# Performance work log

Hardware: AMD Instinct MI355X
Metric: run time of the kernel (lower is better)

## Reference

```python
import jax, jax.numpy as jnp
import numpy as np

N_NODES = 50000
N_EDGES = 800000
IN_DIM, HID_DIM, OUT_DIM = 128, 128, 64


def setup_inputs() -> dict:
    key = jax.random.key(0)
    ks = jax.random.split(key, 8)
    x = jax.random.normal(ks[0], (N_NODES, IN_DIM), dtype=jnp.float32)
    edge_index = jax.random.randint(ks[1], (2, N_EDGES), 0, N_NODES, dtype=jnp.int64)
    # GCNConv uses Glorot weights + zero bias; any random init is fine for a reference
    W1 = jax.random.normal(ks[2], (IN_DIM, HID_DIM), dtype=jnp.float32) / np.sqrt(IN_DIM)
    b1 = jnp.zeros((HID_DIM,), dtype=jnp.float32)
    W2 = jax.random.normal(ks[3], (HID_DIM, OUT_DIM), dtype=jnp.float32) / np.sqrt(HID_DIM)
    b2 = jnp.zeros((OUT_DIM,), dtype=jnp.float32)
    Wfc = jax.random.normal(ks[4], (OUT_DIM, 2), dtype=jnp.float32) / np.sqrt(OUT_DIM)
    bfc = jnp.zeros((2,), dtype=jnp.float32)
    return {"x": x, "edge_index": edge_index, "W1": W1, "b1": b1,
            "W2": W2, "b2": b2, "Wfc": Wfc, "bfc": bfc}


def _gcn_conv(x, src, dst, W, b, n_nodes):
    """PyG GCNConv: out = D^{-1/2} (A+I) D^{-1/2} (x W) + b."""
    xw = x @ W  # [N, F_out] transform before propagation
    ones = jnp.ones(src.shape[0], dtype=xw.dtype)
    deg = jax.ops.segment_sum(ones, dst, num_segments=n_nodes) + 1.0  # +1 for self-loop
    dinv = jax.lax.rsqrt(deg)
    norm = dinv[src] * dinv[dst]  # [E]
    msg = xw[src] * norm[:, None]  # gather + scale: [E, F_out]
    agg = jax.ops.segment_sum(msg, dst, num_segments=n_nodes)  # scatter-add
    agg = agg + xw * (dinv * dinv)[:, None]  # self-loop contribution (norm = 1/deg)
    return agg + b


def reference(x, edge_index, W1, b1, W2, b2, Wfc, bfc):
    n = x.shape[0]
    src, dst = edge_index[0], edge_index[1]
    h = jax.nn.relu(_gcn_conv(x, src, dst, W1, b1, n))
    # dropout is identity in eval mode
    h = _gcn_conv(h, src, dst, W2, b2, n)
    h = h @ Wfc + bfc
    return jax.nn.leaky_relu(h, negative_slope=0.01)
```

## Files before the change

kernel.cpp:

```cpp
#include <hip/hip_runtime.h>
#include <hip/hip_fp16.h>

#define IN_DIM 128
#define HID_DIM 128
#define OUT_DIM 64
#define BINW 128
#define BINSHIFT 7
#define MAXBIN 512
#define CAP 4096
#define CNTSTRIDE 16
#define SC_GRID 512
#define SBUF 2176

typedef _Float16 f16x8 __attribute__((ext_vector_type(8)));
typedef float f32x4 __attribute__((ext_vector_type(4)));

__global__ __launch_bounds__(256) void k_build_gemm(const float* __restrict__ x,
                                                    const float* __restrict__ W,
                                                    __half* __restrict__ xwh,
                                                    const int* __restrict__ src,
                                                    const int* __restrict__ dst,
                                                    int* __restrict__ bin_cnt,
                                                    int* __restrict__ ovf_cnt,
                                                    unsigned int* __restrict__ ovf,
                                                    unsigned int* __restrict__ ebin,
                                                    int N, int E, int nbin) {
    __shared__ union SMem {
        unsigned int wt_raw[8192];
        struct {
            int h[MAXBIN];
            int excl[MAXBIN];
            int base_s[MAXBIN];
            int ps[256];
            unsigned int sb1[SBUF];
            unsigned int sb2[SBUF];
        } sc;
    } smem;
    const int nGemm = (N + 127) >> 7;
    int tid = threadIdx.x;

    if ((int)blockIdx.x < nGemm) {
        char* wb = (char*)smem.wt_raw;
        {
            int kk0 = (tid & 15) * 2;
            int c8  = (tid >> 4) * 8;
#pragma unroll
            for (int i = 0; i < 4; ++i) {
                int kk = i * 32 + kk0;
                const float* w0 = W + (size_t)kk * HID_DIM + c8;
                const float* w1 = w0 + HID_DIM;
                float4 a0 = *(const float4*)w0;
                float4 a1 = *(const float4*)(w0 + 4);
                float4 b0 = *(const float4*)w1;
                float4 b1 = *(const float4*)(w1 + 4);
                float va[8] = {a0.x, a0.y, a0.z, a0.w, a1.x, a1.y, a1.z, a1.w};
                float vb[8] = {b0.x, b0.y, b0.z, b0.w, b1.x, b1.y, b1.z, b1.w};
#pragma unroll
                for (int j = 0; j < 8; ++j) {
                    int col = c8 + j;
                    int byte = (col << 8) + (kk << 1);
                    byte ^= ((col & 7) << 4);
                    *(__half2*)(wb + byte) = __floats2half2_rn(va[j], vb[j]);
                }
            }
        }
        int lane = tid & 63;
        int wv   = tid >> 6;
        int lcol = lane & 15;
        int lk   = (lane >> 4) << 3;
        int swz  = (lcol & 7) << 4;
        int rb   = blockIdx.x * 128 + wv * 32;
        int rows[2];
        const float* xp[2];
#pragma unroll
        for (int r = 0; r < 2; ++r) {
            int row = rb + 16 * r + lcol;
            rows[r] = row;
            if (row > N - 1) row = N - 1;
            xp[r] = x + (size_t)row * IN_DIM + lk;
        }
        f32x4 acc[2][8];
#pragma unroll
        for (int r = 0; r < 2; ++r)
#pragma unroll
            for (int c = 0; c < 8; ++c) acc[r][c] = (f32x4){0.f, 0.f, 0.f, 0.f};

        __syncthreads();

        auto mk = [](float4 f0, float4 f1, f16x8& hi, f16x8& lo) {
            float f[8] = {f0.x, f0.y, f0.z, f0.w, f1.x, f1.y, f1.z, f1.w};
#pragma unroll
            for (int e = 0; e < 8; ++e) {
                _Float16 h = (_Float16)f[e];
                hi[e] = h;
                lo[e] = (_Float16)(f[e] - (float)h);
            }
        };
#pragma unroll
        for (int kc = 0; kc < 4; ++kc) {
            f16x8 xhi[2], xlo[2];
#pragma unroll
            for (int r = 0; r < 2; ++r) {
                float4 f0 = *(const float4*)(xp[r] + kc * 32);
                float4 f1 = *(const float4*)(xp[r] + kc * 32 + 4);
                mk(f0, f1, xhi[r], xlo[r]);
            }
#pragma unroll
            for (int c = 0; c < 8; ++c) {
                int ad = ((c << 12) | (lcol << 8) | ((kc << 6) + (lk << 1))) ^ swz;
                f16x8 wfrag = *(const f16x8*)(wb + ad);
                acc[0][c] = __builtin_amdgcn_mfma_f32_16x16x32_f16(wfrag, xhi[0], acc[0][c], 0, 0, 0);
                acc[0][c] = __builtin_amdgcn_mfma_f32_16x16x32_f16(wfrag, xlo[0], acc[0][c], 0, 0, 0);
                acc[1][c] = __builtin_amdgcn_mfma_f32_16x16x32_f16(wfrag, xhi[1], acc[1][c], 0, 0, 0);
                acc[1][c] = __builtin_amdgcn_mfma_f32_16x16x32_f16(wfrag, xlo[1], acc[1][c], 0, 0, 0);
            }
        }
        int cq = lane >> 4;
#pragma unroll
        for (int r = 0; r < 2; ++r) {
            if (rows[r] < N) {
                uint2* p = (uint2*)(xwh + (size_t)rows[r] * HID_DIM);
#pragma unroll
                for (int c = 0; c < 8; ++c) {
                    union { __half2 h[2]; uint2 u; } pk;
                    pk.h[0] = __floats2half2_rn(acc[r][c].x, acc[r][c].y);
                    pk.h[1] = __floats2half2_rn(acc[r][c].z, acc[r][c].w);
                    p[4 * c + cq] = pk.u;
                }
            }
        }
    } else {
        int sb = blockIdx.x - nGemm;
        int* h = smem.sc.h;
        int* excl = smem.sc.excl;
        int* base_s = smem.sc.base_s;
        int* ps = smem.sc.ps;
        unsigned int* sb1 = smem.sc.sb1;
        unsigned int* sb2 = smem.sc.sb2;
        for (int k = tid; k < MAXBIN; k += 256) h[k] = 0;
        __syncthreads();
        int per = E / SC_GRID;
        int ebeg = sb * per;
        int eend = (sb + 1 == SC_GRID) ? E : ebeg + per;
        for (int i = ebeg + tid; i < eend; i += 256) {
            unsigned int s = (unsigned int)src[i];
            unsigned int d = (unsigned int)dst[i];
            sb1[i - ebeg] = s | (d << 16);
            atomicAdd(&h[d >> BINSHIFT], 1);
        }
        __syncthreads();
        int b0 = 2 * tid, b1 = 2 * tid + 1;
        int c0 = h[b0], c1 = h[b1];
        ps[tid] = c0 + c1;
        __syncthreads();
        for (int off = 1; off < 256; off <<= 1) {
            int v = (tid >= off) ? ps[tid - off] : 0;
            __syncthreads();
            ps[tid] += v;
            __syncthreads();
        }
        int Pprev = (tid > 0) ? ps[tid - 1] : 0;
        excl[b0] = Pprev;
        excl[b1] = Pprev + c0;
        __syncthreads();
        for (int k = tid; k < nbin; k += 256) {
            int c = h[k];
            base_s[k] = (c > 0) ? atomicAdd(&bin_cnt[k * CNTSTRIDE], c) : 0;
            h[k] = 0;
        }
        __syncthreads();
        int tot = eend - ebeg;
        for (int i = tid; i < tot; i += 256) {
            unsigned int p = sb1[i];
            int b = (int)(p >> (16 + BINSHIFT));
            int r = atomicAdd(&h[b], 1);
            sb2[excl[b] + r] = p;
        }
        __syncthreads();
        for (int i = tid; i < tot; i += 256) {
            unsigned int p = sb2[i];
            int b = (int)(p >> (16 + BINSHIFT));
            int g = base_s[b] + (i - excl[b]);
            if (g < CAP) ebin[(size_t)b * CAP + g] = p;
            else ovf[atomicAdd(ovf_cnt, 1)] = p;
        }
    }
}

__global__ __launch_bounds__(256) void k_fill(const unsigned int* __restrict__ ebin,
                                              const int* __restrict__ bin_cnt,
                                              const int* __restrict__ ovf_cnt,
                                              const unsigned int* __restrict__ ovf,
                                              int* __restrict__ row_ptr,
                                              unsigned short* __restrict__ degu,
                                              unsigned short* __restrict__ csr_src,
                                              float* __restrict__ dinv,
                                              const float* __restrict__ W2,
                                              const float* __restrict__ Wfc,
                                              const float* __restrict__ b2,
                                              const float* __restrict__ bfc,
                                              float* __restrict__ Wc,
                                              float* __restrict__ bc,
                                              int N, int nbin) {
    __shared__ int cnt[BINW];
    __shared__ int excl[BINW];
    __shared__ int start[BINW];
    __shared__ unsigned int segl[CAP];
    int k = blockIdx.x;
    int node0 = k * BINW;
    int nn = min(BINW, N - node0);
    int t = threadIdx.x;
    if (t < BINW) cnt[t] = 0;
    int cnt_k = min(bin_cnt[k * CNTSTRIDE], CAP);
    const unsigned int* seg = ebin + (size_t)k * CAP;
    for (int i = t; i < cnt_k; i += 256) segl[i] = seg[i];
    __syncthreads();
    for (int i = t; i < cnt_k; i += 256)
        atomicAdd(&cnt[(segl[i] >> 16) & (BINW - 1)], 1);
    int novf = *ovf_cnt;
    for (int i = t; i < novf; i += 256) {
        unsigned int e = ovf[i];
        if ((int)(e >> (16 + BINSHIFT)) == k)
            atomicAdd(&cnt[(e >> 16) & (BINW - 1)], 1);
    }
    __syncthreads();
    if (t < BINW) excl[t] = (t < nn) ? cnt[t] : 0;
    __syncthreads();
    for (int off = 1; off < BINW; off <<= 1) {
        int u = 0;
        if (t < BINW && t >= off) u = excl[t - off];
        __syncthreads();
        if (t < BINW) excl[t] += u;
        __syncthreads();
    }
    if (t < nn) {
        int deg = cnt[t];
        int e0 = k * CAP + excl[t] - deg;
        start[t] = e0;
        row_ptr[node0 + t] = e0;
        degu[node0 + t] = (unsigned short)deg;
        dinv[node0 + t] = rsqrtf((float)deg + 1.0f);
        cnt[t] = 0;
    }
    __syncthreads();
    for (int i = t; i < cnt_k; i += 256) {
        unsigned int e = segl[i];
        int dl = (e >> 16) & (BINW - 1);
        int slot = start[dl] + atomicAdd(&cnt[dl], 1);
        csr_src[slot] = (unsigned short)(e & 0xffffu);
    }
    for (int i = t; i < novf; i += 256) {
        unsigned int e = ovf[i];
        if ((int)(e >> (16 + BINSHIFT)) == k) {
            int dl = (e >> 16) & (BINW - 1);
            int slot = start[dl] + atomicAdd(&cnt[dl], 1);
            csr_src[slot] = (unsigned short)(e & 0xffffu);
        }
    }
    if (k == 0) {
        int kk = t >> 1, j = t & 1;
        float acc = 0.f;
#pragma unroll 8
        for (int m = 0; m < OUT_DIM; ++m) acc += W2[kk * OUT_DIM + m] * Wfc[m * 2 + j];
        Wc[kk * 2 + j] = acc;
        if (kk == 0) {
            float b = 0.f;
#pragma unroll 8
            for (int m = 0; m < OUT_DIM; ++m) b += b2[m] * Wfc[m * 2 + j];
            bc[j] = b + bfc[j];
        }
    }
}

__global__ __launch_bounds__(256) void k_agg1z(const int* __restrict__ row_ptr,
                                               const unsigned short* __restrict__ degu,
                                               const unsigned short* __restrict__ csr_src,
                                               const float* __restrict__ dinv,
                                               const __half* __restrict__ xwh,
                                               const float* __restrict__ b1,
                                               const float* __restrict__ Wc,
                                               float* __restrict__ z, int N) {
    constexpr int F = HID_DIM;
    constexpr int L = F / 8;
    constexpr int EPW = 64 / L;
    __shared__ float Wcs[HID_DIM * 2];
    int tid = threadIdx.x;
    if (tid < 64) ((float4*)Wcs)[tid] = ((const float4*)Wc)[tid];
    __syncthreads();
    int node = (blockIdx.x * 256 + tid) >> 6;
    if (node >= N) return;
    int lane = tid & 63;
    int sub = lane / L;
    int c   = lane % L;
    int beg = row_ptr[node];
    int end = beg + degu[node];
    float dd = dinv[node];
    uint4 us = *(const uint4*)(xwh + (size_t)node * F + c * 8);
    float4 b1a = *(const float4*)(b1 + c * 8);
    float4 b1b = *(const float4*)(b1 + c * 8 + 4);
    float a0 = 0.f, a1 = 0.f, a2 = 0.f, a3 = 0.f;
    float a4 = 0.f, a5 = 0.f, a6 = 0.f, a7 = 0.f;
    auto acc = [&](uint4 u, float w) {
        float2 v0 = __half22float2(*(__half2*)&u.x);
        float2 v1 = __half22float2(*(__half2*)&u.y);
        float2 v2 = __half22float2(*(__half2*)&u.z);
        float2 v3 = __half22float2(*(__half2*)&u.w);
        a0 = fmaf(v0.x, w, a0); a1 = fmaf(v0.y, w, a1);
        a2 = fmaf(v1.x, w, a2); a3 = fmaf(v1.y, w, a3);
        a4 = fmaf(v2.x, w, a4); a5 = fmaf(v2.y, w, a5);
        a6 = fmaf(v3.x, w, a6); a7 = fmaf(v3.y, w, a7);
    };
    int j = beg + sub;
    for (; j + 3 * EPW < end; j += 4 * EPW) {
        int s0 = csr_src[j];
        int s1 = csr_src[j + EPW];
        int s2 = csr_src[j + 2 * EPW];
        int s3 = csr_src[j + 3 * EPW];
        uint4 u0 = *(const uint4*)(xwh + (size_t)s0 * F + c * 8);
        uint4 u1 = *(const uint4*)(xwh + (size_t)s1 * F + c * 8);
        uint4 u2 = *(const uint4*)(xwh + (size_t)s2 * F + c * 8);
        uint4 u3 = *(const uint4*)(xwh + (size_t)s3 * F + c * 8);
        float w0 = dinv[s0];
        float w1 = dinv[s1];
        float w2 = dinv[s2];
        float w3 = dinv[s3];
        acc(u0, w0); acc(u1, w1); acc(u2, w2); acc(u3, w3);
    }
    for (; j < end; j += EPW) {
        int s = csr_src[j];
        uint4 u = *(const uint4*)(xwh + (size_t)s * F + c * 8);
        acc(u, dinv[s]);
    }
#pragma unroll
    for (int off = L; off < 64; off <<= 1) {
        a0 += __shfl_xor(a0, off); a1 += __shfl_xor(a1, off);
        a2 += __shfl_xor(a2, off); a3 += __shfl_xor(a3, off);
        a4 += __shfl_xor(a4, off); a5 += __shfl_xor(a5, off);
        a6 += __shfl_xor(a6, off); a7 += __shfl_xor(a7, off);
    }
    float2 v0 = __half22float2(*(__half2*)&us.x);
    float2 v1 = __half22float2(*(__half2*)&us.y);
    float2 v2 = __half22float2(*(__half2*)&us.z);
    float2 v3 = __half22float2(*(__half2*)&us.w);
    float h[8];
    h[0] = fmaxf(fmaf(fmaf(v0.x, dd, a0), dd, b1a.x), 0.f);
    h[1] = fmaxf(fmaf(fmaf(v0.y, dd, a1), dd, b1a.y), 0.f);
    h[2] = fmaxf(fmaf(fmaf(v1.x, dd, a2), dd, b1a.z), 0.f);
    h[3] = fmaxf(fmaf(fmaf(v1.y, dd, a3), dd, b1a.w), 0.f);
    h[4] = fmaxf(fmaf(fmaf(v2.x, dd, a4), dd, b1b.x), 0.f);
    h[5] = fmaxf(fmaf(fmaf(v2.y, dd, a5), dd, b1b.y), 0.f);
    h[6] = fmaxf(fmaf(fmaf(v3.x, dd, a6), dd, b1b.z), 0.f);
    h[7] = fmaxf(fmaf(fmaf(v3.y, dd, a7), dd, b1b.w), 0.f);
    float o0 = 0.f, o1 = 0.f;
#pragma unroll
    for (int k = 0; k < 8; ++k) {
        o0 += h[k] * Wcs[(c * 8 + k) * 2 + 0];
        o1 += h[k] * Wcs[(c * 8 + k) * 2 + 1];
    }
#pragma unroll
    for (int off = 1; off < L; off <<= 1) {
        o0 += __shfl_xor(o0, off);
        o1 += __shfl_xor(o1, off);
    }
    if (lane == 0) {
        float2 r; r.x = o0 * dd; r.y = o1 * dd;
        *(float2*)(z + (size_t)node * 2) = r;
    }
}

__global__ __launch_bounds__(256) void k_agg2(const int* __restrict__ row_ptr,
                                              const unsigned short* __restrict__ degu,
                                              const unsigned short* __restrict__ csr_src,
                                              const float* __restrict__ dinv,
                                              const float* __restrict__ z,
                                              const float* __restrict__ bc,
                                              float* __restrict__ out, int N) {
    int tid = threadIdx.x;
    int gwave = (blockIdx.x * 256 + tid) >> 6;
    int lane = tid & 63;
    int grp = lane >> 3, li = lane & 7;
    int node = gwave * 8 + grp;
    if (node >= N) return;
    int beg = row_ptr[node];
    int end = beg + degu[node];
    float s0 = 0.f, s1 = 0.f;
    int j = beg + li;
    for (; j + 8 < end; j += 16) {
        int sa = csr_src[j];
        int sb = csr_src[j + 8];
        float2 za = *(const float2*)(z + (size_t)sa * 2);
        float2 zb = *(const float2*)(z + (size_t)sb * 2);
        s0 += za.x + zb.x; s1 += za.y + zb.y;
    }
    if (j < end) {
        int s = csr_src[j];
        float2 zv = *(const float2*)(z + (size_t)s * 2);
        s0 += zv.x; s1 += zv.y;
    }
#pragma unroll
    for (int off = 1; off < 8; off <<= 1) {
        s0 += __shfl_xor(s0, off);
        s1 += __shfl_xor(s1, off);
    }
    if (li == 0) {
        float2 zs = *(const float2*)(z + (size_t)node * 2);
        float dd = dinv[node];
        float o0 = (s0 + zs.x) * dd + bc[0];
        float o1 = (s1 + zs.y) * dd + bc[1];
        float2 r;
        r.x = o0 > 0.f ? o0 : 0.01f * o0;
        r.y = o1 > 0.f ? o1 : 0.01f * o1;
        *(float2*)(out + (size_t)node * 2) = r;
    }
}

extern "C" void kernel_launch(void* const* d_in, const int* in_sizes, int n_in,
                              void* d_out, int out_size, void* d_ws, size_t ws_size,
                              hipStream_t stream) {
    const float* x   = (const float*)d_in[0];
    const int*   ei  = (const int*)d_in[1];
    const float* W1  = (const float*)d_in[2];
    const float* b1  = (const float*)d_in[3];
    const float* W2  = (const float*)d_in[4];
    const float* b2  = (const float*)d_in[5];
    const float* Wfc = (const float*)d_in[6];
    const float* bfc = (const float*)d_in[7];

    const int N = in_sizes[0] / IN_DIM;
    const int E = in_sizes[1] / 2;
    const int* src = ei;
    const int* dst = ei + E;
    const int nbin = (N + BINW - 1) / BINW;

    char* base = (char*)d_ws;
    size_t off = 0;
    auto take = [&](size_t bytes) { size_t o = off; off = (off + bytes + 255) & ~(size_t)255; return (void*)(base + o); };
    int*    row_ptr  = (int*)take((size_t)N * 4);
    unsigned short* degu = (unsigned short*)take((size_t)N * 2);
    unsigned short* csr_src = (unsigned short*)take((size_t)nbin * CAP * 2);
    int*    bin_cnt  = (int*)take((size_t)(nbin * CNTSTRIDE + CNTSTRIDE) * 4);
    int*    ovf_cnt  = bin_cnt + nbin * CNTSTRIDE;
    unsigned int* ovf = (unsigned int*)take((size_t)E * 4);
    unsigned int* ebin = (unsigned int*)take((size_t)nbin * CAP * 4);
    float*  dinv     = (float*)take((size_t)N * 4);
    __half* xw1h     = (__half*)take((size_t)N * HID_DIM * 2);
    float*  zbuf     = (float*)take((size_t)N * 2 * 4);
    float*  Wc       = (float*)take((size_t)HID_DIM * 2 * 4);
    float*  bc       = (float*)take(2 * 4);

    hipMemsetAsync(bin_cnt, 0, (size_t)(nbin * CNTSTRIDE + CNTSTRIDE) * 4, stream);

    const int nGemm = (N + 127) / 128;
    k_build_gemm<<<nGemm + SC_GRID, 256, 0, stream>>>(x, W1, xw1h, src, dst, bin_cnt,
                                                      ovf_cnt, ovf, ebin, N, E, nbin);
    k_fill<<<nbin, 256, 0, stream>>>(ebin, bin_cnt, ovf_cnt, ovf, row_ptr, degu,
                                     csr_src, dinv, W2, Wfc, b2, bfc, Wc, bc, N, nbin);
    k_agg1z<<<(N + 3) / 4, 256, 0, stream>>>(row_ptr, degu, csr_src, dinv, xw1h, b1, Wc, zbuf, N);
    const int nAgg2 = ((N + 7) / 8 * 64 + 255) / 256;
    k_agg2<<<nAgg2, 256, 0, stream>>>(row_ptr, degu, csr_src, dinv, zbuf, bc, (float*)d_out, N);
}
```

Measured before the change: 159.1 us.

## Fuse CSR fill with layer-1 aggregation and compute degrees via global atomics

```diff
diff --git a/kernel.cpp b/kernel.cpp
--- a/kernel.cpp
+++ b/kernel.cpp
@@ -9,8 +9,8 @@
 #define MAXBIN 512
 #define CAP 4096
 #define CNTSTRIDE 16
-#define SC_GRID 512
-#define SBUF 2176
+#define SC_GRID 256
+#define SBUF 3456
 
 typedef _Float16 f16x8 __attribute__((ext_vector_type(8)));
 typedef float f32x4 __attribute__((ext_vector_type(4)));
@@ -24,6 +24,7 @@
                                                     int* __restrict__ ovf_cnt,
                                                     unsigned int* __restrict__ ovf,
                                                     unsigned int* __restrict__ ebin,
+                                                    int* __restrict__ deg,
                                                     int N, int E, int nbin) {
     __shared__ union SMem {
         unsigned int wt_raw[8192];
@@ -147,6 +148,7 @@
             unsigned int d = (unsigned int)dst[i];
             sb1[i - ebeg] = s | (d << 16);
             atomicAdd(&h[d >> BINSHIFT], 1);
+            atomicAdd(&deg[d], 1);
         }
         __syncthreads();
         int b0 = 2 * tid, b1 = 2 * tid + 1;
@@ -187,25 +189,30 @@
     }
 }
 
-__global__ __launch_bounds__(256) void k_fill(const unsigned int* __restrict__ ebin,
-                                              const int* __restrict__ bin_cnt,
-                                              const int* __restrict__ ovf_cnt,
-                                              const unsigned int* __restrict__ ovf,
-                                              int* __restrict__ row_ptr,
-                                              unsigned short* __restrict__ degu,
-                                              unsigned short* __restrict__ csr_src,
-                                              float* __restrict__ dinv,
-                                              const float* __restrict__ W2,
-                                              const float* __restrict__ Wfc,
-                                              const float* __restrict__ b2,
-                                              const float* __restrict__ bfc,
-                                              float* __restrict__ Wc,
-                                              float* __restrict__ bc,
-                                              int N, int nbin) {
+__global__ __launch_bounds__(256) void k_fillagg(const unsigned int* __restrict__ ebin,
+                                                 const int* __restrict__ bin_cnt,
+                                                 const int* __restrict__ ovf_cnt,
+                                                 const unsigned int* __restrict__ ovf,
+                                                 const int* __restrict__ deg,
+                                                 int* __restrict__ row_ptr,
+                                                 unsigned short* __restrict__ degu,
+                                                 unsigned short* __restrict__ csr_src,
+                                                 float* __restrict__ dinv,
+                                                 const __half* __restrict__ xwh,
+                                                 const float* __restrict__ b1,
+                                                 const float* __restrict__ W2,
+                                                 const float* __restrict__ Wfc,
+                                                 const float* __restrict__ b2,
+                                                 const float* __restrict__ bfc,
+                                                 float* __restrict__ bc,
+                                                 float* __restrict__ z,
+                                                 int N, int nbin) {
     __shared__ int cnt[BINW];
     __shared__ int excl[BINW];
-    __shared__ int start[BINW];
+    __shared__ int start_s[BINW];
     __shared__ unsigned int segl[CAP];
+    __shared__ unsigned short csrl[CAP];
+    __shared__ float Wcs[HID_DIM * 2];
     int k = blockIdx.x;
     int node0 = k * BINW;
     int nn = min(BINW, N - node0);
@@ -214,6 +221,19 @@
     int cnt_k = min(bin_cnt[k * CNTSTRIDE], CAP);
     const unsigned int* seg = ebin + (size_t)k * CAP;
     for (int i = t; i < cnt_k; i += 256) segl[i] = seg[i];
+    {
+        int kk = t >> 1, j = t & 1;
+        float acc = 0.f;
+#pragma unroll 8
+        for (int m = 0; m < OUT_DIM; ++m) acc += W2[kk * OUT_DIM + m] * Wfc[m * 2 + j];
+        Wcs[kk * 2 + j] = acc;
+        if (k == 0 && kk == 0) {
+            float b = 0.f;
+#pragma unroll 8
+            for (int m = 0; m < OUT_DIM; ++m) b += b2[m] * Wfc[m * 2 + j];
+            bc[j] = b + bfc[j];
+        }
+    }
     __syncthreads();
     for (int i = t; i < cnt_k; i += 256)
         atomicAdd(&cnt[(segl[i] >> 16) & (BINW - 1)], 1);
@@ -234,137 +254,117 @@
         __syncthreads();
     }
     if (t < nn) {
-        int deg = cnt[t];
-        int e0 = k * CAP + excl[t] - deg;
-        start[t] = e0;
-        row_ptr[node0 + t] = e0;
-        degu[node0 + t] = (unsigned short)deg;
-        dinv[node0 + t] = rsqrtf((float)deg + 1.0f);
+        int d = cnt[t];
+        int e0 = excl[t] - d;
+        start_s[t] = e0;
+        row_ptr[node0 + t] = k * CAP + e0;
+        degu[node0 + t] = (unsigned short)d;
+        dinv[node0 + t] = rsqrtf((float)d + 1.0f);
         cnt[t] = 0;
     }
     __syncthreads();
     for (int i = t; i < cnt_k; i += 256) {
         unsigned int e = segl[i];
         int dl = (e >> 16) & (BINW - 1);
-        int slot = start[dl] + atomicAdd(&cnt[dl], 1);
-        csr_src[slot] = (unsigned short)(e & 0xffffu);
+        int slot = start_s[dl] + atomicAdd(&cnt[dl], 1);
+        unsigned short sv = (unsigned short)(e & 0xffffu);
+        csrl[slot] = sv;
+        csr_src[(size_t)k * CAP + slot] = sv;
     }
     for (int i = t; i < novf; i += 256) {
         unsigned int e = ovf[i];
         if ((int)(e >> (16 + BINSHIFT)) == k) {
             int dl = (e >> 16) & (BINW - 1);
-            int slot = start[dl] + atomicAdd(&cnt[dl], 1);
-            csr_src[slot] = (unsigned short)(e & 0xffffu);
-        }
-    }
-    if (k == 0) {
-        int kk = t >> 1, j = t & 1;
-        float acc = 0.f;
-#pragma unroll 8
-        for (int m = 0; m < OUT_DIM; ++m) acc += W2[kk * OUT_DIM + m] * Wfc[m * 2 + j];
-        Wc[kk * 2 + j] = acc;
-        if (kk == 0) {
-            float b = 0.f;
-#pragma unroll 8
-            for (int m = 0; m < OUT_DIM; ++m) b += b2[m] * Wfc[m * 2 + j];
-            bc[j] = b + bfc[j];
-        }
-    }
-}
-
-__global__ __launch_bounds__(256) void k_agg1z(const int* __restrict__ row_ptr,
-                                               const unsigned short* __restrict__ degu,
-                                               const unsigned short* __restrict__ csr_src,
-                                               const float* __restrict__ dinv,
-                                               const __half* __restrict__ xwh,
-                                               const float* __restrict__ b1,
-                                               const float* __restrict__ Wc,
-                                               float* __restrict__ z, int N) {
-    constexpr int F = HID_DIM;
-    constexpr int L = F / 8;
-    constexpr int EPW = 64 / L;
-    __shared__ float Wcs[HID_DIM * 2];
-    int tid = threadIdx.x;
-    if (tid < 64) ((float4*)Wcs)[tid] = ((const float4*)Wc)[tid];
+            int slot = start_s[dl] + atomicAdd(&cnt[dl], 1);
+            unsigned short sv = (unsigned short)(e & 0xffffu);
+            csrl[slot] = sv;
+            csr_src[(size_t)k * CAP + slot] = sv;
+        }
+    }
     __syncthreads();
-    int node = (blockIdx.x * 256 + tid) >> 6;
-    if (node >= N) return;
-    int lane = tid & 63;
-    int sub = lane / L;
-    int c   = lane % L;
-    int beg = row_ptr[node];
-    int end = beg + degu[node];
-    float dd = dinv[node];
-    uint4 us = *(const uint4*)(xwh + (size_t)node * F + c * 8);
-    float4 b1a = *(const float4*)(b1 + c * 8);
-    float4 b1b = *(const float4*)(b1 + c * 8 + 4);
-    float a0 = 0.f, a1 = 0.f, a2 = 0.f, a3 = 0.f;
-    float a4 = 0.f, a5 = 0.f, a6 = 0.f, a7 = 0.f;
-    auto acc = [&](uint4 u, float w) {
-        float2 v0 = __half22float2(*(__half2*)&u.x);
-        float2 v1 = __half22float2(*(__half2*)&u.y);
-        float2 v2 = __half22float2(*(__half2*)&u.z);
-        float2 v3 = __half22float2(*(__half2*)&u.w);
-        a0 = fmaf(v0.x, w, a0); a1 = fmaf(v0.y, w, a1);
-        a2 = fmaf(v1.x, w, a2); a3 = fmaf(v1.y, w, a3);
-        a4 = fmaf(v2.x, w, a4); a5 = fmaf(v2.y, w, a5);
-        a6 = fmaf(v3.x, w, a6); a7 = fmaf(v3.y, w, a7);
-    };
-    int j = beg + sub;
-    for (; j + 3 * EPW < end; j += 4 * EPW) {
-        int s0 = csr_src[j];
-        int s1 = csr_src[j + EPW];
-        int s2 = csr_src[j + 2 * EPW];
-        int s3 = csr_src[j + 3 * EPW];
-        uint4 u0 = *(const uint4*)(xwh + (size_t)s0 * F + c * 8);
-        uint4 u1 = *(const uint4*)(xwh + (size_t)s1 * F + c * 8);
-        uint4 u2 = *(const uint4*)(xwh + (size_t)s2 * F + c * 8);
-        uint4 u3 = *(const uint4*)(xwh + (size_t)s3 * F + c * 8);
-        float w0 = dinv[s0];
-        float w1 = dinv[s1];
-        float w2 = dinv[s2];
-        float w3 = dinv[s3];
-        acc(u0, w0); acc(u1, w1); acc(u2, w2); acc(u3, w3);
-    }
-    for (; j < end; j += EPW) {
-        int s = csr_src[j];
-        uint4 u = *(const uint4*)(xwh + (size_t)s * F + c * 8);
-        acc(u, dinv[s]);
-    }
-#pragma unroll
-    for (int off = L; off < 64; off <<= 1) {
-        a0 += __shfl_xor(a0, off); a1 += __shfl_xor(a1, off);
-        a2 += __shfl_xor(a2, off); a3 += __shfl_xor(a3, off);
-        a4 += __shfl_xor(a4, off); a5 += __shfl_xor(a5, off);
-        a6 += __shfl_xor(a6, off); a7 += __shfl_xor(a7, off);
-    }
-    float2 v0 = __half22float2(*(__half2*)&us.x);
-    float2 v1 = __half22float2(*(__half2*)&us.y);
-    float2 v2 = __half22float2(*(__half2*)&us.z);
-    float2 v3 = __half22float2(*(__half2*)&us.w);
-    float h[8];
-    h[0] = fmaxf(fmaf(fmaf(v0.x, dd, a0), dd, b1a.x), 0.f);
-    h[1] = fmaxf(fmaf(fmaf(v0.y, dd, a1), dd, b1a.y), 0.f);
-    h[2] = fmaxf(fmaf(fmaf(v1.x, dd, a2), dd, b1a.z), 0.f);
-    h[3] = fmaxf(fmaf(fmaf(v1.y, dd, a3), dd, b1a.w), 0.f);
-    h[4] = fmaxf(fmaf(fmaf(v2.x, dd, a4), dd, b1b.x), 0.f);
-    h[5] = fmaxf(fmaf(fmaf(v2.y, dd, a5), dd, b1b.y), 0.f);
-    h[6] = fmaxf(fmaf(fmaf(v3.x, dd, a6), dd, b1b.z), 0.f);
-    h[7] = fmaxf(fmaf(fmaf(v3.y, dd, a7), dd, b1b.w), 0.f);
-    float o0 = 0.f, o1 = 0.f;
-#pragma unroll
-    for (int k = 0; k < 8; ++k) {
-        o0 += h[k] * Wcs[(c * 8 + k) * 2 + 0];
-        o1 += h[k] * Wcs[(c * 8 + k) * 2 + 1];
-    }
-#pragma unroll
-    for (int off = 1; off < L; off <<= 1) {
-        o0 += __shfl_xor(o0, off);
-        o1 += __shfl_xor(o1, off);
-    }
-    if (lane == 0) {
-        float2 r; r.x = o0 * dd; r.y = o1 * dd;
-        *(float2*)(z + (size_t)node * 2) = r;
+    int lane = t & 63;
+    int wv4 = t >> 6;
+    int sub = lane >> 4;
+    int c = lane & 15;
+    for (int p = 0; p < BINW / 4; ++p) {
+        int nl = p * 4 + wv4;
+        if (nl >= nn) continue;
+        int node = node0 + nl;
+        int beg = start_s[nl];
+        int dcnt = cnt[nl];
+        int end = beg + dcnt;
+        float dd = rsqrtf((float)dcnt + 1.0f);
+        uint4 us = *(const uint4*)(xwh + (size_t)node * HID_DIM + c * 8);
+        float4 b1a = *(const float4*)(b1 + c * 8);
+        float4 b1b = *(const float4*)(b1 + c * 8 + 4);
+        float a0 = 0.f, a1 = 0.f, a2 = 0.f, a3 = 0.f;
+        float a4 = 0.f, a5 = 0.f, a6 = 0.f, a7 = 0.f;
+        auto accf = [&](uint4 u, float w) {
+            float2 v0 = __half22float2(*(__half2*)&u.x);
+            float2 v1 = __half22float2(*(__half2*)&u.y);
+            float2 v2 = __half22float2(*(__half2*)&u.z);
+            float2 v3 = __half22float2(*(__half2*)&u.w);
+            a0 = fmaf(v0.x, w, a0); a1 = fmaf(v0.y, w, a1);
+            a2 = fmaf(v1.x, w, a2); a3 = fmaf(v1.y, w, a3);
+            a4 = fmaf(v2.x, w, a4); a5 = fmaf(v2.y, w, a5);
+            a6 = fmaf(v3.x, w, a6); a7 = fmaf(v3.y, w, a7);
+        };
+        int j = beg + sub;
+        for (; j + 12 < end; j += 16) {
+            int s0 = csrl[j];
+            int s1 = csrl[j + 4];
+            int s2 = csrl[j + 8];
+            int s3 = csrl[j + 12];
+            uint4 u0 = *(const uint4*)(xwh + (size_t)s0 * HID_DIM + c * 8);
+            uint4 u1 = *(const uint4*)(xwh + (size_t)s1 * HID_DIM + c * 8);
+            uint4 u2 = *(const uint4*)(xwh + (size_t)s2 * HID_DIM + c * 8);
+            uint4 u3 = *(const uint4*)(xwh + (size_t)s3 * HID_DIM + c * 8);
+            float w0 = rsqrtf((float)deg[s0] + 1.0f);
+            float w1 = rsqrtf((float)deg[s1] + 1.0f);
+            float w2 = rsqrtf((float)deg[s2] + 1.0f);
+            float w3 = rsqrtf((float)deg[s3] + 1.0f);
+            accf(u0, w0); accf(u1, w1); accf(u2, w2); accf(u3, w3);
+        }
+        for (; j < end; j += 4) {
+            int s = csrl[j];
+            uint4 u = *(const uint4*)(xwh + (size_t)s * HID_DIM + c * 8);
+            accf(u, rsqrtf((float)deg[s] + 1.0f));
+        }
+#pragma unroll
+        for (int off = 16; off < 64; off <<= 1) {
+            a0 += __shfl_xor(a0, off); a1 += __shfl_xor(a1, off);
+            a2 += __shfl_xor(a2, off); a3 += __shfl_xor(a3, off);
+            a4 += __shfl_xor(a4, off); a5 += __shfl_xor(a5, off);
+            a6 += __shfl_xor(a6, off); a7 += __shfl_xor(a7, off);
+        }
+        float2 v0 = __half22float2(*(__half2*)&us.x);
+        float2 v1 = __half22float2(*(__half2*)&us.y);
+        float2 v2 = __half22float2(*(__half2*)&us.z);
+        float2 v3 = __half22float2(*(__half2*)&us.w);
+        float h[8];
+        h[0] = fmaxf(fmaf(fmaf(v0.x, dd, a0), dd, b1a.x), 0.f);
+        h[1] = fmaxf(fmaf(fmaf(v0.y, dd, a1), dd, b1a.y), 0.f);
+        h[2] = fmaxf(fmaf(fmaf(v1.x, dd, a2), dd, b1a.z), 0.f);
+        h[3] = fmaxf(fmaf(fmaf(v1.y, dd, a3), dd, b1a.w), 0.f);
+        h[4] = fmaxf(fmaf(fmaf(v2.x, dd, a4), dd, b1b.x), 0.f);
+        h[5] = fmaxf(fmaf(fmaf(v2.y, dd, a5), dd, b1b.y), 0.f);
+        h[6] = fmaxf(fmaf(fmaf(v3.x, dd, a6), dd, b1b.z), 0.f);
+        h[7] = fmaxf(fmaf(fmaf(v3.y, dd, a7), dd, b1b.w), 0.f);
+        float o0 = 0.f, o1 = 0.f;
+#pragma unroll
+        for (int m = 0; m < 8; ++m) {
+            o0 += h[m] * Wcs[(c * 8 + m) * 2 + 0];
+            o1 += h[m] * Wcs[(c * 8 + m) * 2 + 1];
+        }
+#pragma unroll
+        for (int off = 1; off < 16; off <<= 1) {
+            o0 += __shfl_xor(o0, off);
+            o1 += __shfl_xor(o1, off);
+        }
+        if (lane == 0) {
+            float2 r; r.x = o0 * dd; r.y = o1 * dd;
+            *(float2*)(z + (size_t)node * 2) = r;
+        }
     }
 }
 
@@ -440,22 +440,23 @@
     unsigned short* csr_src = (unsigned short*)take((size_t)nbin * CAP * 2);
     int*    bin_cnt  = (int*)take((size_t)(nbin * CNTSTRIDE + CNTSTRIDE) * 4);
     int*    ovf_cnt  = bin_cnt + nbin * CNTSTRIDE;
+    int*    deg      = (int*)take((size_t)N * 4);
     unsigned int* ovf = (unsigned int*)take((size_t)E * 4);
     unsigned int* ebin = (unsigned int*)take((size_t)nbin * CAP * 4);
     float*  dinv     = (float*)take((size_t)N * 4);
     __half* xw1h     = (__half*)take((size_t)N * HID_DIM * 2);
     float*  zbuf     = (float*)take((size_t)N * 2 * 4);
-    float*  Wc       = (float*)take((size_t)HID_DIM * 2 * 4);
     float*  bc       = (float*)take(2 * 4);
 
-    hipMemsetAsync(bin_cnt, 0, (size_t)(nbin * CNTSTRIDE + CNTSTRIDE) * 4, stream);
+    size_t zspan = (char*)(deg + N) - (char*)bin_cnt;
+    hipMemsetAsync(bin_cnt, 0, zspan, stream);
 
     const int nGemm = (N + 127) / 128;
     k_build_gemm<<<nGemm + SC_GRID, 256, 0, stream>>>(x, W1, xw1h, src, dst, bin_cnt,
-                                                      ovf_cnt, ovf, ebin, N, E, nbin);
-    k_fill<<<nbin, 256, 0, stream>>>(ebin, bin_cnt, ovf_cnt, ovf, row_ptr, degu,
-                                     csr_src, dinv, W2, Wfc, b2, bfc, Wc, bc, N, nbin);
-    k_agg1z<<<(N + 3) / 4, 256, 0, stream>>>(row_ptr, degu, csr_src, dinv, xw1h, b1, Wc, zbuf, N);
+                                                      ovf_cnt, ovf, ebin, deg, N, E, nbin);
+    k_fillagg<<<nbin, 256, 0, stream>>>(ebin, bin_cnt, ovf_cnt, ovf, deg, row_ptr, degu,
+                                        csr_src, dinv, xw1h, b1, W2, Wfc, b2, bfc, bc,
+                                        zbuf, N, nbin);
     const int nAgg2 = ((N + 7) / 8 * 64 + 255) / 256;
     k_agg2<<<nAgg2, 256, 0, stream>>>(row_ptr, degu, csr_src, dinv, zbuf, bc, (float*)d_out, N);
 }
```

Result: slower. 225.0 us (+41.4%).
